# Kernel optimization log

Hardware: AMD Instinct MI355X
Metric: run time of the kernel (lower is better)

Reference implementation:

```python
import jax, jax.numpy as jnp
import numpy as np
import math

B, S, D = 4, 1024, 1024
H, DK, DV = 16, 64, 64
MAX_REL = 32  # use_neg_dist=True -> vocab = 2*MAX_REL+1


def setup_inputs() -> dict:
    key = jax.random.key(0)
    ks = jax.random.split(key, 13)
    sc = 0.02
    return {
        "key": jax.random.normal(ks[0], (B, S, D), jnp.float32),
        "value": jax.random.normal(ks[1], (B, S, D), jnp.float32),
        "query": jax.random.normal(ks[2], (B, S, D), jnp.float32),
        "Wk": jax.random.normal(ks[3], (D, H * DK), jnp.float32) * sc,
        "bk": jnp.zeros((H * DK,), jnp.float32),
        "Wq": jax.random.normal(ks[4], (D, H * DK), jnp.float32) * sc,
        "bq": jnp.zeros((H * DK,), jnp.float32),
        "Wv": jax.random.normal(ks[5], (D, H * DV), jnp.float32) * sc,
        "bv": jnp.zeros((H * DV,), jnp.float32),
        "Wo": jax.random.normal(ks[6], (H * DV, D), jnp.float32) * sc,
        "bo": jnp.zeros((D,), jnp.float32),
        "emb_k": jax.random.normal(ks[7], (2 * MAX_REL + 1, DK), jnp.float32) * sc,
        "emb_v": jax.random.normal(ks[8], (2 * MAX_REL + 1, DV), jnp.float32) * sc,
    }


def reference(key, value, query, Wk, bk, Wq, bq, Wv, bv, Wo, bo, emb_k, emb_v):
    # project and split heads -> [B, H, S, d]
    def shape(x, d):
        return x.reshape(B, S, H, d).transpose(0, 2, 1, 3)

    k = shape(key @ Wk + bk, DK)
    v = shape(value @ Wv + bv, DV)
    q = shape(query @ Wq + bq, DK)

    # relative position ids: [S, S] in [0, 2*MAX_REL]
    r = jnp.arange(S)
    rel_idx = jnp.clip(r[None, :] - r[:, None], -MAX_REL, MAX_REL) + MAX_REL
    rel_k = emb_k[rel_idx]  # [S, S, DK]
    rel_v = emb_v[rel_idx]  # [S, S, DV]

    q = q / math.sqrt(DK)
    # content scores + relative-key scores (relative_matmul with transpose=True)
    scores = jnp.einsum("bhqd,bhkd->bhqk", q, k) + jnp.einsum("bhqd,qkd->bhqk", q, rel_k)
    attn = jax.nn.softmax(scores.astype(jnp.float32), axis=-1).astype(q.dtype)

    # context + relative-value contribution (relative_matmul with transpose=False)
    ctx = jnp.einsum("bhqk,bhkd->bhqd", attn, v) + jnp.einsum("bhqk,qkd->bhqd", attn, rel_v)
    ctx = ctx.transpose(0, 2, 1, 3).reshape(B, S, H * DV)
    final_output = ctx @ Wo + bo
    return final_output, attn
```

## Files before the change

kernel.cpp:

```cpp
#include <hip/hip_runtime.h>
#include <hip/hip_bf16.h>

#define B_ 4
#define S_ 1024
#define D_ 1024
#define H_ 16

typedef unsigned short u16;
typedef __bf16 bf16x8 __attribute__((ext_vector_type(8)));
typedef float f32x4 __attribute__((ext_vector_type(4)));

__device__ inline u16 f2bf(float f) {
    __bf16 h = (__bf16)f;
    return __builtin_bit_cast(u16, h);
}
__device__ inline float bf2f(u16 u) {
    unsigned int x = ((unsigned int)u) << 16;
    return __builtin_bit_cast(float, x);
}
__device__ inline void gl_lds16(const u16* g, u16* lbase) {
    __builtin_amdgcn_global_load_lds(
        (const __attribute__((address_space(1))) unsigned int*)g,
        (__attribute__((address_space(3))) unsigned int*)lbase, 16, 0, 0);
}
__device__ inline int xcd_swz(int bid, int nwg) {
    int cpx = nwg >> 3;
    return (bid & 7) * cpx + (bid >> 3);
}
__device__ inline bf16x8 frag_swz(const u16* lds, int row, int chunk) {
    int off = (row << 6) + ((chunk ^ (row & 7)) << 3);
    return *(const bf16x8*)(lds + off);
}
__device__ inline bf16x8 frag_p(const u16* lds, int row, int chunk) {
    int off = row * 72 + (chunk << 3);
    return *(const bf16x8*)(lds + off);
}
__device__ inline f32x4 mfma16(bf16x8 a, bf16x8 b, f32x4 c) {
    return __builtin_amdgcn_mfma_f32_16x16x32_bf16(a, b, c, 0, 0, 0);
}
__device__ inline void bar() {
    asm volatile("s_waitcnt lgkmcnt(0)\n\ts_barrier" ::: "memory");
}
__device__ inline void wait_vm0() {
    asm volatile("s_waitcnt vmcnt(0)" ::: "memory");
    __builtin_amdgcn_sched_barrier(0);
}
__device__ inline void wait_vm4() {
    asm volatile("s_waitcnt vmcnt(4)" ::: "memory");
    __builtin_amdgcn_sched_barrier(0);
}
__device__ inline void wait_vm8() {
    asm volatile("s_waitcnt vmcnt(8)" ::: "memory");
    __builtin_amdgcn_sched_barrier(0);
}
__device__ inline void wait_vm16() {
    asm volatile("s_waitcnt vmcnt(16)" ::: "memory");
    __builtin_amdgcn_sched_barrier(0);
}
__device__ inline void wait_vm20() {
    asm volatile("s_waitcnt vmcnt(20)" ::: "memory");
    __builtin_amdgcn_sched_barrier(0);
}
__device__ inline void wait_lgkm0() {
    asm volatile("s_waitcnt lgkmcnt(0)" ::: "memory");
    __builtin_amdgcn_sched_barrier(0);
}

__global__ __launch_bounds__(256) void cast3_kernel(
    const float* __restrict__ q, const float* __restrict__ k, const float* __restrict__ v,
    u16* __restrict__ xq, u16* __restrict__ xk, u16* __restrict__ xv) {
    int bid = blockIdx.x;
    int which = bid >> 12;
    int t = bid & 4095;
    const float* src = which == 0 ? q : (which == 1 ? k : v);
    u16* dst = which == 0 ? xq : (which == 1 ? xk : xv);
    int i = (t * 256 + threadIdx.x) * 4;
    float4 val = *(const float4*)(src + i);
    ushort4 o;
    o.x = f2bf(val.x); o.y = f2bf(val.y); o.z = f2bf(val.z); o.w = f2bf(val.w);
    *(ushort4*)(dst + i) = o;
}

__global__ __launch_bounds__(256) void tcast4_kernel(
    const float* __restrict__ Wq, const float* __restrict__ Wk,
    const float* __restrict__ Wv, const float* __restrict__ Wo,
    u16* __restrict__ wt, u16* __restrict__ wot) {
    __shared__ float tile[32][33];
    int z = blockIdx.z;
    const float* src = z == 0 ? Wq : (z == 1 ? Wk : (z == 2 ? Wv : Wo));
    u16* dst = z < 3 ? wt + (size_t)z * 1024 * 1024 : wot;
    int bx = blockIdx.x, by = blockIdx.y;
    int tx = threadIdx.x, ty = threadIdx.y;
    int x = bx * 32 + tx;
    for (int i = ty; i < 32; i += 8)
        tile[i][tx] = src[(size_t)(by * 32 + i) * 1024 + x];
    __syncthreads();
    int col = by * 32 + tx;
    for (int i = ty; i < 32; i += 8)
        dst[(size_t)(bx * 32 + i) * 1024 + col] = f2bf(tile[tx][i]);
}

__device__ inline void gemm_core(const u16* __restrict__ A, const u16* __restrict__ Bt,
                                 int m0, int n0, u16* lsA, u16* lsB, f32x4 acc[4][4]) {
    int tid = threadIdx.x, lane = tid & 63, wave = tid >> 6;
    int quad = lane >> 4, l16 = lane & 15;
    int wm = wave >> 1, wn = wave & 1;
    f32x4 z = {0.0f, 0.0f, 0.0f, 0.0f};
    for (int mi = 0; mi < 4; mi++)
        for (int ni = 0; ni < 4; ni++) acc[mi][ni] = z;
    auto stg = [&](int k0, int b) {
        const u16* abase = A + (size_t)m0 * 1024 + k0;
        const u16* bbase = Bt + (size_t)n0 * 1024 + k0;
#pragma unroll
        for (int j = 0; j < 4; j++) {
            int C = (wave * 4 + j) * 64 + lane;
            int row = C >> 3, c = C & 7;
            int sw = (c ^ (row & 7)) << 3;
            gl_lds16(abase + (size_t)row * 1024 + sw, lsA + b * 8192 + (wave * 4 + j) * 512);
            gl_lds16(bbase + (size_t)row * 1024 + sw, lsB + b * 8192 + (wave * 4 + j) * 512);
        }
    };
    stg(0, 0);
#pragma unroll 1
    for (int it = 0; it < 16; it++) {
        if (it < 15) {
            stg((it + 1) * 64, (it + 1) & 1);
            wait_vm8();
        } else {
            wait_vm0();
        }
        bar();
        const u16* cA = lsA + (it & 1) * 8192;
        const u16* cB = lsB + (it & 1) * 8192;
        for (int s = 0; s < 2; s++) {
            bf16x8 af[4], bfv[4];
            for (int mi = 0; mi < 4; mi++) af[mi] = frag_swz(cA, wm * 64 + mi * 16 + l16, s * 4 + quad);
            for (int ni = 0; ni < 4; ni++) bfv[ni] = frag_swz(cB, wn * 64 + ni * 16 + l16, s * 4 + quad);
            for (int mi = 0; mi < 4; mi++)
                for (int ni = 0; ni < 4; ni++)
                    acc[mi][ni] = mfma16(af[mi], bfv[ni], acc[mi][ni]);
        }
        bar();
    }
}

__global__ __launch_bounds__(256) void gemm_proj_kernel(
    const u16* __restrict__ xq, const u16* __restrict__ xk, const u16* __restrict__ xv,
    const u16* __restrict__ wt,
    const float* __restrict__ bq, const float* __restrict__ bk, const float* __restrict__ bv,
    u16* __restrict__ qb, u16* __restrict__ kb, u16* __restrict__ vtb) {
    __shared__ __align__(16) u16 lsA[2 * 128 * 64];
    __shared__ __align__(16) u16 lsB[2 * 128 * 64];
    int bid = xcd_swz(blockIdx.x, 768);
    int which = bid >> 8;
    int t = bid & 255;
    int m0 = (t >> 3) * 128, n0 = (t & 7) * 128;
    const u16* A = which == 0 ? xq : (which == 1 ? xk : xv);
    const u16* Bt = wt + (size_t)which * 1024 * 1024;
    const float* bias = which == 0 ? bq : (which == 1 ? bk : bv);
    f32x4 acc[4][4];
    gemm_core(A, Bt, m0, n0, lsA, lsB, acc);
    int tid = threadIdx.x, lane = tid & 63, wave = tid >> 6;
    int quad = lane >> 4, l16 = lane & 15;
    int wm = wave >> 1, wn = wave & 1;
    for (int mi = 0; mi < 4; mi++) {
        int rbase = m0 + wm * 64 + mi * 16 + quad * 4;
        int b = rbase >> 10, s0 = rbase & 1023;
        for (int ni = 0; ni < 4; ni++) {
            int n = n0 + wn * 64 + ni * 16 + l16;
            int h = n >> 6, d = n & 63;
            float bsv = bias[n];
            if (which == 2) {
                ushort4 pk;
                pk.x = f2bf(acc[mi][ni][0] + bsv);
                pk.y = f2bf(acc[mi][ni][1] + bsv);
                pk.z = f2bf(acc[mi][ni][2] + bsv);
                pk.w = f2bf(acc[mi][ni][3] + bsv);
                *(ushort4*)(vtb + ((size_t)(b * H_ + h) * 64 + d) * 1024 + s0) = pk;
            } else {
                u16* outp = (which == 0) ? qb : kb;
                float scl = (which == 0) ? 0.125f : 1.0f;
                for (int r = 0; r < 4; r++) {
                    int s = s0 + r;
                    outp[((size_t)(b * H_ + h) * 1024 + s) * 64 + d] = f2bf((acc[mi][ni][r] + bsv) * scl);
                }
            }
        }
    }
}

__global__ __launch_bounds__(256) void gemm_final_kernel(const u16* __restrict__ ctxb,
                                                         const u16* __restrict__ wot,
                                                         const float* __restrict__ bo,
                                                         float* __restrict__ out) {
    __shared__ __align__(16) u16 lsA[2 * 128 * 64];
    __shared__ __align__(16) u16 lsB[2 * 128 * 64];
    int bid = xcd_swz(blockIdx.x, 256);
    int m0 = (bid >> 3) * 128, n0 = (bid & 7) * 128;
    f32x4 acc[4][4];
    gemm_core(ctxb, wot, m0, n0, lsA, lsB, acc);
    int tid = threadIdx.x, lane = tid & 63, wave = tid >> 6;
    int quad = lane >> 4, l16 = lane & 15;
    int wm = wave >> 1, wn = wave & 1;
    for (int mi = 0; mi < 4; mi++)
        for (int ni = 0; ni < 4; ni++) {
            int n = n0 + wn * 64 + ni * 16 + l16;
            float bsv = bo[n];
            for (int r = 0; r < 4; r++) {
                int row = m0 + wm * 64 + mi * 16 + quad * 4 + r;
                out[(size_t)row * 1024 + n] = acc[mi][ni][r] + bsv;
            }
        }
}

__global__ __launch_bounds__(256, 2) void attn_kernel(
    const u16* __restrict__ qb, const u16* __restrict__ kb, const u16* __restrict__ vtb,
    const float* __restrict__ emb_k, const float* __restrict__ emb_v,
    float* __restrict__ attn_out, u16* __restrict__ ctxb) {
    __shared__ __align__(16) u16 kvbuf[4][64 * 64];
    __shared__ __align__(16) u16 pbuf[64 * 72];
    __shared__ __align__(16) u16 wqbuf[64 * 72];
    __shared__ __align__(16) u16 qrel[64 * 68];

    int bid = xcd_swz(blockIdx.x, 1024);
    int qt = bid & 15, bh = bid >> 4;
    int tid = threadIdx.x, lane = tid & 63, wave = tid >> 6;
    int quad = lane >> 4, l16 = lane & 15;
    int mrow = wave * 16;

    const u16* qbase = qb + ((size_t)bh * 1024 + qt * 64) * 64;
    const u16* kbh = kb + (size_t)bh * 1024 * 64;
    const u16* vbh = vtb + (size_t)bh * 64 * 1024;

    auto stage = [&](const u16* src, int srcStride, u16* dst) {
#pragma unroll
        for (int j = 0; j < 2; j++) {
            int C = (wave * 2 + j) * 64 + lane;
            int row = C >> 3, c = C & 7;
            gl_lds16(src + (size_t)row * srcStride + ((c ^ (row & 7)) << 3),
                     dst + (wave * 2 + j) * 512);
        }
    };
    auto stage128 = [&](const u16* src, u16* dst) {
#pragma unroll
        for (int j = 0; j < 4; j++) {
            int C = (wave * 4 + j) * 64 + lane;
            int row = C >> 3, c = C & 7;
            gl_lds16(src + (size_t)row * 64 + ((c ^ (row & 7)) << 3),
                     dst + (wave * 4 + j) * 512);
        }
    };

    stage(qbase, 64, wqbuf);
    for (int i = tid; i < 65 * 64; i += 256) {
        int j = i >> 6, d = i & 63;
        pbuf[(j << 6) + ((((d >> 3) ^ (j & 7)) << 3) | (d & 7))] = f2bf(emb_k[i]);
    }
    wait_vm0();
    bar();

    {
        bf16x8 a0 = frag_swz(wqbuf, mrow + l16, quad);
        bf16x8 a1 = frag_swz(wqbuf, mrow + l16, 4 + quad);
#pragma unroll
        for (int ni = 0; ni < 5; ni++) {
            int rr = ni * 16 + l16;
            rr = rr > 64 ? 64 : rr;
            f32x4 a = {0.0f, 0.0f, 0.0f, 0.0f};
            a = mfma16(a0, frag_swz(pbuf, rr, quad), a);
            a = mfma16(a1, frag_swz(pbuf, rr, 4 + quad), a);
            int j = ni * 16 + l16;
            if (j < 65) {
#pragma unroll
                for (int r = 0; r < 4; r++)
                    qrel[(mrow + quad * 4 + r) * 68 + j] = f2bf(a[r]);
            }
        }
    }
    bf16x8 aq0 = frag_swz(wqbuf, mrow + l16, quad);
    bf16x8 aq1 = frag_swz(wqbuf, mrow + l16, 4 + quad);
    bar();

    float rel_l[4], rel_r[4];
#pragma unroll
    for (int r = 0; r < 4; r++) {
        int ql = mrow + quad * 4 + r;
        rel_l[r] = bf2f(qrel[ql * 68 + 0]);
        rel_r[r] = bf2f(qrel[ql * 68 + 64]);
    }
    stage128(kbh, kvbuf[0]);
    {
        unsigned int* wz = (unsigned int*)wqbuf;
        for (int i = lane; i < 16 * 36; i += 64) wz[mrow * 36 + i] = 0u;
    }

    float l_acc[4] = {0.0f, 0.0f, 0.0f, 0.0f};

#pragma unroll 1
    for (int it = 0; it < 8; it++) {
        if (it < 7) {
            stage128(kbh + (size_t)(it + 1) * 8192, (it & 1) ? kvbuf[0] : kvbuf[2]);
            wait_vm4();
        } else {
            wait_vm0();
        }
        bar();
        const u16* kl = (it & 1) ? kvbuf[2] : kvbuf[0];
        int cls = (it * 128 + 127 <= qt * 64 - 32) ? 0 : ((it * 128 >= qt * 64 + 95) ? 2 : 1);
        __builtin_amdgcn_s_setprio(1);
        if (cls == 0) {
#pragma unroll
            for (int ni = 0; ni < 8; ni++) {
                f32x4 a = {0.0f, 0.0f, 0.0f, 0.0f};
                a = mfma16(aq0, frag_swz(kl, ni * 16 + l16, quad), a);
                a = mfma16(aq1, frag_swz(kl, ni * 16 + l16, 4 + quad), a);
#pragma unroll
                for (int r = 0; r < 4; r++) l_acc[r] += __expf(a[r] + rel_l[r]);
            }
        } else if (cls == 2) {
#pragma unroll
            for (int ni = 0; ni < 8; ni++) {
                f32x4 a = {0.0f, 0.0f, 0.0f, 0.0f};
                a = mfma16(aq0, frag_swz(kl, ni * 16 + l16, quad), a);
                a = mfma16(aq1, frag_swz(kl, ni * 16 + l16, 4 + quad), a);
#pragma unroll
                for (int r = 0; r < 4; r++) l_acc[r] += __expf(a[r] + rel_r[r]);
            }
        } else {
#pragma unroll
            for (int ni = 0; ni < 8; ni++) {
                f32x4 a = {0.0f, 0.0f, 0.0f, 0.0f};
                a = mfma16(aq0, frag_swz(kl, ni * 16 + l16, quad), a);
                a = mfma16(aq1, frag_swz(kl, ni * 16 + l16, 4 + quad), a);
#pragma unroll
                for (int r = 0; r < 4; r++) {
                    int ql = mrow + quad * 4 + r;
                    int qg = qt * 64 + ql;
                    int kg = it * 128 + ni * 16 + l16;
                    int jj = kg - qg;
                    jj = jj < -32 ? -32 : (jj > 32 ? 32 : jj);
                    l_acc[r] += __expf(a[r] + bf2f(qrel[ql * 68 + jj + 32]));
                }
            }
        }
        __builtin_amdgcn_s_setprio(0);
        bar();
    }

    float rl[4];
#pragma unroll
    for (int r = 0; r < 4; r++) {
        float l = l_acc[r];
        l += __shfl_xor(l, 1);
        l += __shfl_xor(l, 2);
        l += __shfl_xor(l, 4);
        l += __shfl_xor(l, 8);
        rl[r] = 1.0f / l;
    }
    float wl[4] = {0.0f, 0.0f, 0.0f, 0.0f};
    float wr[4] = {0.0f, 0.0f, 0.0f, 0.0f};
    f32x4 ctx[4];
    {
        f32x4 z = {0.0f, 0.0f, 0.0f, 0.0f};
#pragma unroll
        for (int ni = 0; ni < 4; ni++) ctx[ni] = z;
    }
    float* attn_bh = attn_out + (size_t)bh * 1024 * 1024;

    stage(kbh, 64, kvbuf[0]);
    stage(vbh, 1024, kvbuf[2]);
    wait_vm0();
    bar();
#pragma unroll 1
    for (int kt = 0; kt < 16; kt++) {
        if (kt < 15) {
            stage(kbh + (size_t)(kt + 1) * 4096, 64, (kt & 1) ? kvbuf[0] : kvbuf[1]);
            stage(vbh + (kt + 1) * 64, 1024, (kt & 1) ? kvbuf[2] : kvbuf[3]);
        }
        if (kt == 0) wait_vm4();
        else if (kt == 15) wait_vm16();
        else wait_vm20();
        bar();
        const u16* kl = (kt & 1) ? kvbuf[1] : kvbuf[0];
        const u16* vl = (kt & 1) ? kvbuf[3] : kvbuf[2];
        f32x4 sc[4];
        __builtin_amdgcn_s_setprio(1);
#pragma unroll
        for (int ni = 0; ni < 4; ni++) {
            f32x4 a = {0.0f, 0.0f, 0.0f, 0.0f};
            a = mfma16(aq0, frag_swz(kl, ni * 16 + l16, quad), a);
            a = mfma16(aq1, frag_swz(kl, ni * 16 + l16, 4 + quad), a);
            sc[ni] = a;
        }
        __builtin_amdgcn_s_setprio(0);
        int cls = (kt <= qt - 2) ? 0 : ((kt >= qt + 2) ? 2 : 1);
        if (cls == 0) {
#pragma unroll
            for (int ni = 0; ni < 4; ni++)
#pragma unroll
                for (int r = 0; r < 4; r++) {
                    int ql = mrow + quad * 4 + r;
                    int qg = qt * 64 + ql;
                    int kg = kt * 64 + ni * 16 + l16;
                    float p = __expf(sc[ni][r] + rel_l[r]) * rl[r];
                    __builtin_nontemporal_store(p, &attn_bh[(size_t)qg * 1024 + kg]);
                    pbuf[ql * 72 + ni * 16 + l16] = f2bf(p);
                    wl[r] += p;
                }
        } else if (cls == 2) {
#pragma unroll
            for (int ni = 0; ni < 4; ni++)
#pragma unroll
                for (int r = 0; r < 4; r++) {
                    int ql = mrow + quad * 4 + r;
                    int qg = qt * 64 + ql;
                    int kg = kt * 64 + ni * 16 + l16;
                    float p = __expf(sc[ni][r] + rel_r[r]) * rl[r];
                    __builtin_nontemporal_store(p, &attn_bh[(size_t)qg * 1024 + kg]);
                    pbuf[ql * 72 + ni * 16 + l16] = f2bf(p);
                    wr[r] += p;
                }
        } else {
#pragma unroll
            for (int ni = 0; ni < 4; ni++)
#pragma unroll
                for (int r = 0; r < 4; r++) {
                    int ql = mrow + quad * 4 + r;
                    int qg = qt * 64 + ql;
                    int kg = kt * 64 + ni * 16 + l16;
                    int jj = kg - qg;
                    int jc = jj < -32 ? -32 : (jj > 32 ? 32 : jj);
                    float p = __expf(sc[ni][r] + bf2f(qrel[ql * 68 + jc + 32])) * rl[r];
                    __builtin_nontemporal_store(p, &attn_bh[(size_t)qg * 1024 + kg]);
                    u16 pb = f2bf(p);
                    pbuf[ql * 72 + ni * 16 + l16] = pb;
                    if (jj <= -32) wl[r] += p;
                    else if (jj >= 32) wr[r] += p;
                    else wqbuf[ql * 72 + jj + 32] = pb;
                }
        }
        wait_lgkm0();
        __builtin_amdgcn_s_setprio(1);
#pragma unroll
        for (int s2 = 0; s2 < 2; s2++) {
            bf16x8 af = frag_p(pbuf, mrow + l16, s2 * 4 + quad);
#pragma unroll
            for (int ni = 0; ni < 4; ni++)
                ctx[ni] = mfma16(af, frag_swz(vl, ni * 16 + l16, s2 * 4 + quad), ctx[ni]);
        }
        __builtin_amdgcn_s_setprio(0);
        bar();
    }

#pragma unroll
    for (int r = 0; r < 4; r++) {
        wl[r] += __shfl_xor(wl[r], 1); wl[r] += __shfl_xor(wl[r], 2);
        wl[r] += __shfl_xor(wl[r], 4); wl[r] += __shfl_xor(wl[r], 8);
        wr[r] += __shfl_xor(wr[r], 1); wr[r] += __shfl_xor(wr[r], 2);
        wr[r] += __shfl_xor(wr[r], 4); wr[r] += __shfl_xor(wr[r], 8);
    }
    if (l16 == 0) {
#pragma unroll
        for (int r = 0; r < 4; r++)
            wqbuf[(mrow + quad * 4 + r) * 72] = f2bf(wl[r]);
    }
    u16* evt = kvbuf[0];
    for (int i = tid; i < 4096; i += 256) {
        int j = i >> 6, d = i & 63;
        evt[d * 72 + j] = f2bf(emb_v[i]);
    }
    __syncthreads();
#pragma unroll
    for (int s2 = 0; s2 < 2; s2++) {
        bf16x8 af = frag_p(wqbuf, mrow + l16, s2 * 4 + quad);
#pragma unroll
        for (int ni = 0; ni < 4; ni++)
            ctx[ni] = mfma16(af, frag_p(evt, ni * 16 + l16, s2 * 4 + quad), ctx[ni]);
    }
#pragma unroll
    for (int ni = 0; ni < 4; ni++) {
        float ev = emb_v[64 * 64 + ni * 16 + l16];
#pragma unroll
        for (int r = 0; r < 4; r++) ctx[ni][r] += wr[r] * ev;
    }

    int b = bh >> 4, h = bh & 15;
#pragma unroll
    for (int ni = 0; ni < 4; ni++)
#pragma unroll
        for (int r = 0; r < 4; r++) {
            int ql = mrow + quad * 4 + r;
            int sg = qt * 64 + ql;
            ctxb[((size_t)b * 1024 + sg) * 1024 + h * 64 + ni * 16 + l16] = f2bf(ctx[ni][r]);
        }
}

extern "C" void kernel_launch(void* const* d_in, const int* in_sizes, int n_in,
                              void* d_out, int out_size, void* d_ws, size_t ws_size,
                              hipStream_t stream) {
    const float* key_f   = (const float*)d_in[0];
    const float* value_f = (const float*)d_in[1];
    const float* query_f = (const float*)d_in[2];
    const float* Wk = (const float*)d_in[3];
    const float* bk = (const float*)d_in[4];
    const float* Wq = (const float*)d_in[5];
    const float* bq = (const float*)d_in[6];
    const float* Wv = (const float*)d_in[7];
    const float* bv = (const float*)d_in[8];
    const float* Wo = (const float*)d_in[9];
    const float* bo = (const float*)d_in[10];
    const float* emb_k = (const float*)d_in[11];
    const float* emb_v = (const float*)d_in[12];

    char* ws = (char*)d_ws;
    const size_t MB = 1024 * 1024;
    u16* xq   = (u16*)(ws + 0 * MB);
    u16* xk   = (u16*)(ws + 8 * MB);
    u16* xv   = (u16*)(ws + 16 * MB);
    u16* wt   = (u16*)(ws + 24 * MB);
    u16* wot  = (u16*)(ws + 30 * MB);
    u16* qb   = (u16*)(ws + 32 * MB);
    u16* kb   = (u16*)(ws + 40 * MB);
    u16* vtb  = (u16*)(ws + 48 * MB);
    u16* ctxb = (u16*)(ws + 56 * MB);

    float* out0 = (float*)d_out;
    float* attn = out0 + (size_t)4 * 1024 * 1024;

    cast3_kernel<<<12288, 256, 0, stream>>>(query_f, key_f, value_f, xq, xk, xv);
    dim3 tg(32, 32, 4), tb(32, 8);
    tcast4_kernel<<<tg, tb, 0, stream>>>(Wq, Wk, Wv, Wo, wt, wot);
    gemm_proj_kernel<<<768, 256, 0, stream>>>(xq, xk, xv, wt, bq, bk, bv, qb, kb, vtb);
    attn_kernel<<<1024, 256, 0, stream>>>(qb, kb, vtb, emb_k, emb_v, attn, ctxb);
    gemm_final_kernel<<<256, 256, 0, stream>>>(ctxb, wot, bo, out0);
}
```

Measured before the change: 481.5 us.

## Load K/V MFMA fragments directly from global memory, drop LDS staging

The attention kernel no longer double-buffers K and V tiles through LDS with global_load_lds and barriers. Each wave now reads its MFMA operand fragments straight from global memory, and the freed LDS lets launch bounds rise to 4 blocks per CU. The input cast and weight transpose-cast kernels are also merged into one launch, and the classified branches are folded together. In exchange, each wave issues redundant uncoalesced global reads, and the strided V^T reads may put more pressure on L2 and global memory latency.

```diff
diff --git a/kernel.cpp b/kernel.cpp
--- a/kernel.cpp
+++ b/kernel.cpp
@@ -35,6 +35,9 @@
     int off = row * 72 + (chunk << 3);
     return *(const bf16x8*)(lds + off);
 }
+__device__ inline bf16x8 gfrag(const u16* g) {
+    return *(const bf16x8*)g;
+}
 __device__ inline f32x4 mfma16(bf16x8 a, bf16x8 b, f32x4 c) {
     return __builtin_amdgcn_mfma_f32_16x16x32_bf16(a, b, c, 0, 0, 0);
 }
@@ -45,59 +48,49 @@
     asm volatile("s_waitcnt vmcnt(0)" ::: "memory");
     __builtin_amdgcn_sched_barrier(0);
 }
-__device__ inline void wait_vm4() {
-    asm volatile("s_waitcnt vmcnt(4)" ::: "memory");
-    __builtin_amdgcn_sched_barrier(0);
-}
 __device__ inline void wait_vm8() {
     asm volatile("s_waitcnt vmcnt(8)" ::: "memory");
     __builtin_amdgcn_sched_barrier(0);
 }
-__device__ inline void wait_vm16() {
-    asm volatile("s_waitcnt vmcnt(16)" ::: "memory");
-    __builtin_amdgcn_sched_barrier(0);
-}
-__device__ inline void wait_vm20() {
-    asm volatile("s_waitcnt vmcnt(20)" ::: "memory");
-    __builtin_amdgcn_sched_barrier(0);
-}
 __device__ inline void wait_lgkm0() {
     asm volatile("s_waitcnt lgkmcnt(0)" ::: "memory");
     __builtin_amdgcn_sched_barrier(0);
 }
 
-__global__ __launch_bounds__(256) void cast3_kernel(
+__global__ __launch_bounds__(256) void prep_kernel(
     const float* __restrict__ q, const float* __restrict__ k, const float* __restrict__ v,
-    u16* __restrict__ xq, u16* __restrict__ xk, u16* __restrict__ xv) {
-    int bid = blockIdx.x;
-    int which = bid >> 12;
-    int t = bid & 4095;
-    const float* src = which == 0 ? q : (which == 1 ? k : v);
-    u16* dst = which == 0 ? xq : (which == 1 ? xk : xv);
-    int i = (t * 256 + threadIdx.x) * 4;
-    float4 val = *(const float4*)(src + i);
-    ushort4 o;
-    o.x = f2bf(val.x); o.y = f2bf(val.y); o.z = f2bf(val.z); o.w = f2bf(val.w);
-    *(ushort4*)(dst + i) = o;
-}
-
-__global__ __launch_bounds__(256) void tcast4_kernel(
     const float* __restrict__ Wq, const float* __restrict__ Wk,
     const float* __restrict__ Wv, const float* __restrict__ Wo,
+    u16* __restrict__ xq, u16* __restrict__ xk, u16* __restrict__ xv,
     u16* __restrict__ wt, u16* __restrict__ wot) {
     __shared__ float tile[32][33];
-    int z = blockIdx.z;
-    const float* src = z == 0 ? Wq : (z == 1 ? Wk : (z == 2 ? Wv : Wo));
-    u16* dst = z < 3 ? wt + (size_t)z * 1024 * 1024 : wot;
-    int bx = blockIdx.x, by = blockIdx.y;
-    int tx = threadIdx.x, ty = threadIdx.y;
-    int x = bx * 32 + tx;
-    for (int i = ty; i < 32; i += 8)
-        tile[i][tx] = src[(size_t)(by * 32 + i) * 1024 + x];
-    __syncthreads();
-    int col = by * 32 + tx;
-    for (int i = ty; i < 32; i += 8)
-        dst[(size_t)(bx * 32 + i) * 1024 + col] = f2bf(tile[tx][i]);
+    int bid = blockIdx.x;
+    int tid = threadIdx.x;
+    if (bid < 12288) {
+        int which = bid >> 12;
+        int t = bid & 4095;
+        const float* src = which == 0 ? q : (which == 1 ? k : v);
+        u16* dst = which == 0 ? xq : (which == 1 ? xk : xv);
+        int i = (t * 256 + tid) * 4;
+        float4 val = *(const float4*)(src + i);
+        ushort4 o;
+        o.x = f2bf(val.x); o.y = f2bf(val.y); o.z = f2bf(val.z); o.w = f2bf(val.w);
+        *(ushort4*)(dst + i) = o;
+    } else {
+        int t2 = bid - 12288;
+        int z = t2 >> 10, rem = t2 & 1023;
+        int by = rem >> 5, bx = rem & 31;
+        int tx = tid & 31, ty = tid >> 5;
+        const float* src = z == 0 ? Wq : (z == 1 ? Wk : (z == 2 ? Wv : Wo));
+        u16* dst = z < 3 ? wt + (size_t)z * 1024 * 1024 : wot;
+        int x = bx * 32 + tx;
+        for (int i = ty; i < 32; i += 8)
+            tile[i][tx] = src[(size_t)(by * 32 + i) * 1024 + x];
+        __syncthreads();
+        int col = by * 32 + tx;
+        for (int i = ty; i < 32; i += 8)
+            dst[(size_t)(bx * 32 + i) * 1024 + col] = f2bf(tile[tx][i]);
+    }
 }
 
 __device__ inline void gemm_core(const u16* __restrict__ A, const u16* __restrict__ Bt,
@@ -213,11 +206,10 @@
         }
 }
 
-__global__ __launch_bounds__(256, 2) void attn_kernel(
+__global__ __launch_bounds__(256, 4) void attn_kernel(
     const u16* __restrict__ qb, const u16* __restrict__ kb, const u16* __restrict__ vtb,
     const float* __restrict__ emb_k, const float* __restrict__ emb_v,
     float* __restrict__ attn_out, u16* __restrict__ ctxb) {
-    __shared__ __align__(16) u16 kvbuf[4][64 * 64];
     __shared__ __align__(16) u16 pbuf[64 * 72];
     __shared__ __align__(16) u16 wqbuf[64 * 72];
     __shared__ __align__(16) u16 qrel[64 * 68];
@@ -232,26 +224,15 @@
     const u16* kbh = kb + (size_t)bh * 1024 * 64;
     const u16* vbh = vtb + (size_t)bh * 64 * 1024;
 
-    auto stage = [&](const u16* src, int srcStride, u16* dst) {
+    {
 #pragma unroll
         for (int j = 0; j < 2; j++) {
             int C = (wave * 2 + j) * 64 + lane;
             int row = C >> 3, c = C & 7;
-            gl_lds16(src + (size_t)row * srcStride + ((c ^ (row & 7)) << 3),
-                     dst + (wave * 2 + j) * 512);
-        }
-    };
-    auto stage128 = [&](const u16* src, u16* dst) {
-#pragma unroll
-        for (int j = 0; j < 4; j++) {
-            int C = (wave * 4 + j) * 64 + lane;
-            int row = C >> 3, c = C & 7;
-            gl_lds16(src + (size_t)row * 64 + ((c ^ (row & 7)) << 3),
-                     dst + (wave * 4 + j) * 512);
-        }
-    };
-
-    stage(qbase, 64, wqbuf);
+            gl_lds16(qbase + (size_t)row * 64 + ((c ^ (row & 7)) << 3),
+                     wqbuf + (wave * 2 + j) * 512);
+        }
+    }
     for (int i = tid; i < 65 * 64; i += 256) {
         int j = i >> 6, d = i & 63;
         pbuf[(j << 6) + ((((d >> 3) ^ (j & 7)) << 3) | (d & 7))] = f2bf(emb_k[i]);
@@ -288,7 +269,6 @@
         rel_l[r] = bf2f(qrel[ql * 68 + 0]);
         rel_r[r] = bf2f(qrel[ql * 68 + 64]);
     }
-    stage128(kbh, kvbuf[0]);
     {
         unsigned int* wz = (unsigned int*)wqbuf;
         for (int i = lane; i < 16 * 36; i += 64) wz[mrow * 36 + i] = 0u;
@@ -298,53 +278,39 @@
 
 #pragma unroll 1
     for (int it = 0; it < 8; it++) {
-        if (it < 7) {
-            stage128(kbh + (size_t)(it + 1) * 8192, (it & 1) ? kvbuf[0] : kvbuf[2]);
-            wait_vm4();
-        } else {
-            wait_vm0();
-        }
-        bar();
-        const u16* kl = (it & 1) ? kvbuf[2] : kvbuf[0];
         int cls = (it * 128 + 127 <= qt * 64 - 32) ? 0 : ((it * 128 >= qt * 64 + 95) ? 2 : 1);
         __builtin_amdgcn_s_setprio(1);
-        if (cls == 0) {
+        if (cls == 1) {
 #pragma unroll
             for (int ni = 0; ni < 8; ni++) {
+                int kg = it * 128 + ni * 16 + l16;
+                const u16* kp = kbh + (size_t)kg * 64;
                 f32x4 a = {0.0f, 0.0f, 0.0f, 0.0f};
-                a = mfma16(aq0, frag_swz(kl, ni * 16 + l16, quad), a);
-                a = mfma16(aq1, frag_swz(kl, ni * 16 + l16, 4 + quad), a);
-#pragma unroll
-                for (int r = 0; r < 4; r++) l_acc[r] += __expf(a[r] + rel_l[r]);
-            }
-        } else if (cls == 2) {
-#pragma unroll
-            for (int ni = 0; ni < 8; ni++) {
-                f32x4 a = {0.0f, 0.0f, 0.0f, 0.0f};
-                a = mfma16(aq0, frag_swz(kl, ni * 16 + l16, quad), a);
-                a = mfma16(aq1, frag_swz(kl, ni * 16 + l16, 4 + quad), a);
-#pragma unroll
-                for (int r = 0; r < 4; r++) l_acc[r] += __expf(a[r] + rel_r[r]);
-            }
-        } else {
-#pragma unroll
-            for (int ni = 0; ni < 8; ni++) {
-                f32x4 a = {0.0f, 0.0f, 0.0f, 0.0f};
-                a = mfma16(aq0, frag_swz(kl, ni * 16 + l16, quad), a);
-                a = mfma16(aq1, frag_swz(kl, ni * 16 + l16, 4 + quad), a);
+                a = mfma16(aq0, gfrag(kp + quad * 8), a);
+                a = mfma16(aq1, gfrag(kp + (4 + quad) * 8), a);
 #pragma unroll
                 for (int r = 0; r < 4; r++) {
                     int ql = mrow + quad * 4 + r;
                     int qg = qt * 64 + ql;
-                    int kg = it * 128 + ni * 16 + l16;
                     int jj = kg - qg;
                     jj = jj < -32 ? -32 : (jj > 32 ? 32 : jj);
                     l_acc[r] += __expf(a[r] + bf2f(qrel[ql * 68 + jj + 32]));
                 }
             }
+        } else {
+            const float* relc = (cls == 0) ? rel_l : rel_r;
+#pragma unroll
+            for (int ni = 0; ni < 8; ni++) {
+                int kg = it * 128 + ni * 16 + l16;
+                const u16* kp = kbh + (size_t)kg * 64;
+                f32x4 a = {0.0f, 0.0f, 0.0f, 0.0f};
+                a = mfma16(aq0, gfrag(kp + quad * 8), a);
+                a = mfma16(aq1, gfrag(kp + (4 + quad) * 8), a);
+#pragma unroll
+                for (int r = 0; r < 4; r++) l_acc[r] += __expf(a[r] + relc[r]);
+            }
         }
         __builtin_amdgcn_s_setprio(0);
-        bar();
     }
 
     float rl[4];
@@ -367,60 +333,22 @@
     }
     float* attn_bh = attn_out + (size_t)bh * 1024 * 1024;
 
-    stage(kbh, 64, kvbuf[0]);
-    stage(vbh, 1024, kvbuf[2]);
-    wait_vm0();
-    bar();
 #pragma unroll 1
     for (int kt = 0; kt < 16; kt++) {
-        if (kt < 15) {
-            stage(kbh + (size_t)(kt + 1) * 4096, 64, (kt & 1) ? kvbuf[0] : kvbuf[1]);
-            stage(vbh + (kt + 1) * 64, 1024, (kt & 1) ? kvbuf[2] : kvbuf[3]);
-        }
-        if (kt == 0) wait_vm4();
-        else if (kt == 15) wait_vm16();
-        else wait_vm20();
-        bar();
-        const u16* kl = (kt & 1) ? kvbuf[1] : kvbuf[0];
-        const u16* vl = (kt & 1) ? kvbuf[3] : kvbuf[2];
         f32x4 sc[4];
         __builtin_amdgcn_s_setprio(1);
 #pragma unroll
         for (int ni = 0; ni < 4; ni++) {
+            int kg = kt * 64 + ni * 16 + l16;
+            const u16* kp = kbh + (size_t)kg * 64;
             f32x4 a = {0.0f, 0.0f, 0.0f, 0.0f};
-            a = mfma16(aq0, frag_swz(kl, ni * 16 + l16, quad), a);
-            a = mfma16(aq1, frag_swz(kl, ni * 16 + l16, 4 + quad), a);
+            a = mfma16(aq0, gfrag(kp + quad * 8), a);
+            a = mfma16(aq1, gfrag(kp + (4 + quad) * 8), a);
             sc[ni] = a;
         }
         __builtin_amdgcn_s_setprio(0);
         int cls = (kt <= qt - 2) ? 0 : ((kt >= qt + 2) ? 2 : 1);
-        if (cls == 0) {
-#pragma unroll
-            for (int ni = 0; ni < 4; ni++)
-#pragma unroll
-                for (int r = 0; r < 4; r++) {
-                    int ql = mrow + quad * 4 + r;
-                    int qg = qt * 64 + ql;
-                    int kg = kt * 64 + ni * 16 + l16;
-                    float p = __expf(sc[ni][r] + rel_l[r]) * rl[r];
-                    __builtin_nontemporal_store(p, &attn_bh[(size_t)qg * 1024 + kg]);
-                    pbuf[ql * 72 + ni * 16 + l16] = f2bf(p);
-                    wl[r] += p;
-                }
-        } else if (cls == 2) {
-#pragma unroll
-            for (int ni = 0; ni < 4; ni++)
-#pragma unroll
-                for (int r = 0; r < 4; r++) {
-                    int ql = mrow + quad * 4 + r;
-                    int qg = qt * 64 + ql;
-                    int kg = kt * 64 + ni * 16 + l16;
-                    float p = __expf(sc[ni][r] + rel_r[r]) * rl[r];
-                    __builtin_nontemporal_store(p, &attn_bh[(size_t)qg * 1024 + kg]);
-                    pbuf[ql * 72 + ni * 16 + l16] = f2bf(p);
-                    wr[r] += p;
-                }
-        } else {
+        if (cls == 1) {
 #pragma unroll
             for (int ni = 0; ni < 4; ni++)
 #pragma unroll
@@ -438,6 +366,21 @@
                     else if (jj >= 32) wr[r] += p;
                     else wqbuf[ql * 72 + jj + 32] = pb;
                 }
+        } else {
+            const float* relc = (cls == 0) ? rel_l : rel_r;
+            float* wacc = (cls == 0) ? wl : wr;
+#pragma unroll
+            for (int ni = 0; ni < 4; ni++)
+#pragma unroll
+                for (int r = 0; r < 4; r++) {
+                    int ql = mrow + quad * 4 + r;
+                    int qg = qt * 64 + ql;
+                    int kg = kt * 64 + ni * 16 + l16;
+                    float p = __expf(sc[ni][r] + relc[r]) * rl[r];
+                    __builtin_nontemporal_store(p, &attn_bh[(size_t)qg * 1024 + kg]);
+                    pbuf[ql * 72 + ni * 16 + l16] = f2bf(p);
+                    wacc[r] += p;
+                }
         }
         wait_lgkm0();
         __builtin_amdgcn_s_setprio(1);
@@ -445,11 +388,12 @@
         for (int s2 = 0; s2 < 2; s2++) {
             bf16x8 af = frag_p(pbuf, mrow + l16, s2 * 4 + quad);
 #pragma unroll
-            for (int ni = 0; ni < 4; ni++)
-                ctx[ni] = mfma16(af, frag_swz(vl, ni * 16 + l16, s2 * 4 + quad), ctx[ni]);
+            for (int ni = 0; ni < 4; ni++) {
+                const u16* vp = vbh + (size_t)(ni * 16 + l16) * 1024 + kt * 64 + (s2 * 4 + quad) * 8;
+                ctx[ni] = mfma16(af, gfrag(vp), ctx[ni]);
+            }
         }
         __builtin_amdgcn_s_setprio(0);
-        bar();
     }
 
 #pragma unroll
@@ -459,12 +403,13 @@
         wr[r] += __shfl_xor(wr[r], 1); wr[r] += __shfl_xor(wr[r], 2);
         wr[r] += __shfl_xor(wr[r], 4); wr[r] += __shfl_xor(wr[r], 8);
     }
+    bar();
     if (l16 == 0) {
 #pragma unroll
         for (int r = 0; r < 4; r++)
             wqbuf[(mrow + quad * 4 + r) * 72] = f2bf(wl[r]);
     }
-    u16* evt = kvbuf[0];
+    u16* evt = pbuf;
     for (int i = tid; i < 4096; i += 256) {
         int j = i >> 6, d = i & 63;
         evt[d * 72 + j] = f2bf(emb_v[i]);
@@ -527,9 +472,8 @@
     float* out0 = (float*)d_out;
     float* attn = out0 + (size_t)4 * 1024 * 1024;
 
-    cast3_kernel<<<12288, 256, 0, stream>>>(query_f, key_f, value_f, xq, xk, xv);
-    dim3 tg(32, 32, 4), tb(32, 8);
-    tcast4_kernel<<<tg, tb, 0, stream>>>(Wq, Wk, Wv, Wo, wt, wot);
+    prep_kernel<<<16384, 256, 0, stream>>>(query_f, key_f, value_f, Wq, Wk, Wv, Wo,
+                                           xq, xk, xv, wt, wot);
     gemm_proj_kernel<<<768, 256, 0, stream>>>(xq, xk, xv, wt, bq, bk, bv, qb, kb, vtb);
     attn_kernel<<<1024, 256, 0, stream>>>(qb, kb, vtb, emb_k, emb_v, attn, ctxb);
     gemm_final_kernel<<<256, 256, 0, stream>>>(ctxb, wot, bo, out0);
```

Result: slower. 588.5 us (+22.2%).
